# Kernel optimization log

Measured on AMD Instinct MI355X. Metric: run time of the kernel, lower is better.

Reference implementation:

```python
import jax, jax.numpy as jnp
import numpy as np

DIM = 1024
HEADS = 16
HEAD_DIM = DIM // HEADS
SCALE = HEAD_DIM ** -0.5


def setup_inputs() -> dict:
    key = jax.random.key(0)
    k1, k2, k3, k4 = jax.random.split(key, 4)
    x = jax.random.normal(k1, (2, 2048, DIM), dtype=jnp.float32)
    s = DIM ** -0.5
    qkv_w = jax.random.normal(k2, (3 * DIM, DIM), dtype=jnp.float32) * s
    proj_w = jax.random.normal(k3, (DIM, DIM), dtype=jnp.float32) * s
    proj_b = jax.random.normal(k4, (DIM,), dtype=jnp.float32) * 0.01
    return {"x": x, "qkv_w": qkv_w, "proj_w": proj_w, "proj_b": proj_b}


def reference(x, qkv_w, proj_w, proj_b):
    B, N, C = x.shape
    # qkv: Linear(dim, 3*dim) with torch convention y = x @ W^T
    qkv = jnp.einsum('bnc,dc->bnd', x, qkv_w)
    qkv = qkv.reshape(B, N, 3, HEADS, HEAD_DIM).transpose(2, 0, 3, 1, 4)
    q, k, v = qkv[0], qkv[1], qkv[2]           # [B, H, N, Dh]
    attn = jnp.einsum('bhnd,bhmd->bhnm', q, k) * SCALE
    attn = jax.nn.softmax(attn, axis=-1)
    out = jnp.einsum('bhnm,bhmd->bhnd', attn, v)  # [B, H, N, Dh]
    out = out.transpose(0, 2, 1, 3).reshape(B, N, C)
    out = jnp.einsum('bnc,dc->bnd', out, proj_w) + proj_b
    return out
```

## Files before the change

kernel.cpp:

```cpp
#include <hip/hip_runtime.h>
#include <cmath>


namespace {
constexpr int kDim   = 1024;
constexpr int kHeads = 16;
constexpr int kHd    = 64;
constexpr int kB     = 2;
constexpr int kN     = 2048;
constexpr int kM     = kB * kN;
constexpr float kScale = 0.125f;
constexpr int kP = 72;
}

typedef __attribute__((ext_vector_type(8))) short bf16x8;
typedef __attribute__((ext_vector_type(4))) float f32x4;

__device__ inline unsigned short f2bf(float x) {
  union { float f; unsigned u; } un; un.f = x;
  unsigned r = un.u + 0x7fffu + ((un.u >> 16) & 1u);
  return (unsigned short)(r >> 16);
}
__device__ inline unsigned pack2bf(float x, float y) {
  return (unsigned)f2bf(x) | ((unsigned)f2bf(y) << 16);
}
__device__ inline void gl_lds16(const short* g, short* l) {
  __builtin_amdgcn_global_load_lds(
      (const __attribute__((address_space(1))) unsigned*)g,
      (__attribute__((address_space(3))) unsigned*)l, 16, 0, 0);
}

__global__ __launch_bounds__(256) void cvt_kernel(const float* __restrict__ src,
                                                  short* __restrict__ dst) {
  const int i = (blockIdx.x * 256 + threadIdx.x) * 8;
  float4 a = *(const float4*)&src[i];
  float4 b = *(const float4*)&src[i + 4];
  bf16x8 o = {(short)f2bf(a.x), (short)f2bf(a.y), (short)f2bf(a.z), (short)f2bf(a.w),
              (short)f2bf(b.x), (short)f2bf(b.y), (short)f2bf(b.z), (short)f2bf(b.w)};
  *(bf16x8*)&dst[i] = o;
}

__global__ __launch_bounds__(256, 2) void mm_qkv_kernel(
    const short* __restrict__ A16, const short* __restrict__ W16,
    short* __restrict__ q16, short* __restrict__ k16, short* __restrict__ vT16) {
  __shared__ short smem[2 * 128 * 64];
  short* As = smem;
  short* Bs = smem + 128 * 64;
  const int tid  = threadIdx.x;
  const int w    = tid >> 6;
  const int lane = tid & 63;
  const int quad = lane >> 4;
  const int k15  = lane & 15;
  const int m0   = blockIdx.x * 128;
  const int seg  = blockIdx.y >> 3;
  const int nt0  = (blockIdx.y & 7) << 7;
  const int wrow0 = seg * 1024 + nt0;
  const int wm = (w >> 1) * 64;
  const int wn = (w & 1) * 64;
  const int lrow   = lane >> 3;
  const int lchunk = (lane & 7) ^ lrow;

  f32x4 acc[4][4];
#pragma unroll
  for (int i = 0; i < 4; ++i)
#pragma unroll
    for (int j = 0; j < 4; ++j) acc[i][j] = (f32x4){0.f, 0.f, 0.f, 0.f};

  for (int kt = 0; kt < 1024; kt += 64) {
    __syncthreads();
#pragma unroll
    for (int p = 0; p < 4; ++p) {
      const int r0 = p * 32 + w * 8;
      gl_lds16(&A16[(long)(m0 + r0 + lrow) * 1024 + kt + lchunk * 8], &As[r0 * 64]);
      gl_lds16(&W16[(long)(wrow0 + r0 + lrow) * 1024 + kt + lchunk * 8], &Bs[r0 * 64]);
    }
    __syncthreads();
#pragma unroll
    for (int ks = 0; ks < 2; ++ks) {
      bf16x8 af[4], bf[4];
#pragma unroll
      for (int t = 0; t < 4; ++t) {
        const int Ra = wm + t * 16 + k15;
        af[t] = *(const bf16x8*)&As[Ra * 64 + (((ks << 2) + quad) ^ (Ra & 7)) * 8];
        const int Rb = wn + t * 16 + k15;
        bf[t] = *(const bf16x8*)&Bs[Rb * 64 + (((ks << 2) + quad) ^ (Rb & 7)) * 8];
      }
#pragma unroll
      for (int mt = 0; mt < 4; ++mt)
#pragma unroll
        for (int nt = 0; nt < 4; ++nt)
          acc[mt][nt] = __builtin_amdgcn_mfma_f32_16x16x32_bf16(
              af[mt], bf[nt], acc[mt][nt], 0, 0, 0);
    }
  }

  if (seg < 2) {
    short* dst = (seg == 0) ? q16 : k16;
    const float sc = (seg == 0) ? kScale : 1.0f;
#pragma unroll
    for (int nt = 0; nt < 4; ++nt) {
      const int dl = nt0 + wn + nt * 16 + k15;
      const int h  = dl >> 6;
      const int dh = dl & 63;
#pragma unroll
      for (int mt = 0; mt < 4; ++mt) {
#pragma unroll
        for (int r = 0; r < 4; ++r) {
          const int ml = m0 + wm + mt * 16 + quad * 4 + r;
          const int b  = ml >> 11;
          const int n  = ml & 2047;
          dst[(((long)(b * kHeads + h) * kN) + n) * kHd + dh] =
              (short)f2bf(acc[mt][nt][r] * sc);
        }
      }
    }
  } else {
    __syncthreads();
    short* Tw = smem + w * 16 * kP;
#pragma unroll
    for (int nt = 0; nt < 4; ++nt) {
#pragma unroll
      for (int mt = 0; mt < 4; ++mt) {
        uint2 pk;
        pk.x = pack2bf(acc[mt][nt][0], acc[mt][nt][1]);
        pk.y = pack2bf(acc[mt][nt][2], acc[mt][nt][3]);
        *(uint2*)&Tw[k15 * kP + mt * 16 + quad * 4] = pk;
      }
#pragma unroll
      for (int i = 0; i < 2; ++i) {
        const int idx  = i * 64 + lane;
        const int trow = idx >> 3;
        const int tch  = idx & 7;
        bf16x8 row = *(const bf16x8*)&Tw[trow * kP + tch * 8];
        const int vcol = nt0 + wn + nt * 16 + trow;
        const int h  = vcol >> 6;
        const int dh = vcol & 63;
        const int m  = m0 + wm + tch * 8;
        const int b  = m >> 11;
        const int n  = m & 2047;
        *(bf16x8*)&vT16[(((long)(b * kHeads + h) * kHd) + dh) * kN + n] = row;
      }
    }
  }
}

__global__ __launch_bounds__(256, 2) void mm_proj_kernel(
    const short* __restrict__ A16, const short* __restrict__ B16,
    const float* __restrict__ bias, float* __restrict__ out) {
  __shared__ short As[128 * 64];
  __shared__ short Bs[128 * 64];
  const int tid  = threadIdx.x;
  const int w    = tid >> 6;
  const int lane = tid & 63;
  const int quad = lane >> 4;
  const int k15  = lane & 15;
  const int m0 = blockIdx.x * 128;
  const int n0 = blockIdx.y * 128;
  const int wm = (w >> 1) * 64;
  const int wn = (w & 1) * 64;
  const int lrow   = lane >> 3;
  const int lchunk = (lane & 7) ^ lrow;

  f32x4 acc[4][4];
#pragma unroll
  for (int i = 0; i < 4; ++i)
#pragma unroll
    for (int j = 0; j < 4; ++j) acc[i][j] = (f32x4){0.f, 0.f, 0.f, 0.f};

  for (int kt = 0; kt < 1024; kt += 64) {
    __syncthreads();
#pragma unroll
    for (int p = 0; p < 4; ++p) {
      const int r0 = p * 32 + w * 8;
      gl_lds16(&A16[(long)(m0 + r0 + lrow) * 1024 + kt + lchunk * 8], &As[r0 * 64]);
      gl_lds16(&B16[(long)(n0 + r0 + lrow) * 1024 + kt + lchunk * 8], &Bs[r0 * 64]);
    }
    __syncthreads();
#pragma unroll
    for (int ks = 0; ks < 2; ++ks) {
      bf16x8 af[4], bf[4];
#pragma unroll
      for (int t = 0; t < 4; ++t) {
        const int Ra = wm + t * 16 + k15;
        af[t] = *(const bf16x8*)&As[Ra * 64 + (((ks << 2) + quad) ^ (Ra & 7)) * 8];
        const int Rb = wn + t * 16 + k15;
        bf[t] = *(const bf16x8*)&Bs[Rb * 64 + (((ks << 2) + quad) ^ (Rb & 7)) * 8];
      }
#pragma unroll
      for (int mt = 0; mt < 4; ++mt)
#pragma unroll
        for (int nt = 0; nt < 4; ++nt)
          acc[mt][nt] = __builtin_amdgcn_mfma_f32_16x16x32_bf16(
              af[mt], bf[nt], acc[mt][nt], 0, 0, 0);
    }
  }

#pragma unroll
  for (int nt = 0; nt < 4; ++nt) {
    const int d = n0 + wn + nt * 16 + k15;
    const float bb = bias[d];
#pragma unroll
    for (int mt = 0; mt < 4; ++mt) {
#pragma unroll
      for (int r = 0; r < 4; ++r) {
        const int m = m0 + wm + mt * 16 + quad * 4 + r;
        out[(long)m * 1024 + d] = acc[mt][nt][r] + bb;
      }
    }
  }
}

__global__ __launch_bounds__(256, 2) void attn_kernel(
    const short* __restrict__ q16, const short* __restrict__ k16,
    const short* __restrict__ vT16, short* __restrict__ ao16) {
  __shared__ short Ks[128 * 64];
  __shared__ short Vs[64 * 128];
  __shared__ short Ps[4 * 32 * kP];

  const int tid  = threadIdx.x;
  const int w    = tid >> 6;
  const int lane = tid & 63;
  const int quad = lane >> 4;
  const int k15  = lane & 15;
  const int lrow  = lane >> 3;
  const int lch8  = lane & 7;
  const int lrow4 = lane >> 4;
  const int lch16 = lane & 15;
  const int bufIdx = blockIdx.z * kHeads + blockIdx.y;
  const long base  = (long)bufIdx * kN * kHd;

  bf16x8 qf[2][2];
#pragma unroll
  for (int qt = 0; qt < 2; ++qt) {
    const long qr = base + (long)(blockIdx.x * 128 + w * 32 + qt * 16 + k15) * kHd;
#pragma unroll
    for (int ks = 0; ks < 2; ++ks)
      qf[qt][ks] = *(const bf16x8*)&q16[qr + ks * 32 + quad * 8];
  }

  f32x4 accO[2][4];
#pragma unroll
  for (int qt = 0; qt < 2; ++qt)
#pragma unroll
    for (int d = 0; d < 4; ++d) accO[qt][d] = (f32x4){0.f, 0.f, 0.f, 0.f};
  float lsum[2][4] = {{0.f,0.f,0.f,0.f},{0.f,0.f,0.f,0.f}};
  short* pw = Ps + w * 32 * kP;

  for (int kt = 0; kt < kN / 128; ++kt) {
    __syncthreads();
    {
      const short* kg = k16 + base + (long)kt * 128 * kHd;
      const short* vg = vT16 + base + kt * 128;
#pragma unroll
      for (int c = 0; c < 4; ++c) {
        const int r0 = w * 32 + c * 8;
        gl_lds16(kg + (long)(r0 + lrow) * kHd + (lch8 ^ lrow) * 8, &Ks[r0 * 64]);
      }
#pragma unroll
      for (int c = 0; c < 4; ++c) {
        const int r0v = w * 16 + c * 4;
        gl_lds16(vg + (long)(r0v + lrow4) * kN + (lch16 ^ ((c * 4 + lrow4) & 15)) * 8,
                 &Vs[r0v * 128]);
      }
    }
    __syncthreads();

#pragma unroll
    for (int h2 = 0; h2 < 2; ++h2) {
      f32x4 sc[2][4];
#pragma unroll
      for (int t = 0; t < 4; ++t) {
        const int row = h2 * 64 + t * 16 + k15;
        bf16x8 kb0 = *(const bf16x8*)&Ks[row * 64 + ((quad) ^ (k15 & 7)) * 8];
        bf16x8 kb1 = *(const bf16x8*)&Ks[row * 64 + ((4 + quad) ^ (k15 & 7)) * 8];
#pragma unroll
        for (int qt = 0; qt < 2; ++qt) {
          f32x4 z = {0.f, 0.f, 0.f, 0.f};
          z = __builtin_amdgcn_mfma_f32_16x16x32_bf16(qf[qt][0], kb0, z, 0, 0, 0);
          z = __builtin_amdgcn_mfma_f32_16x16x32_bf16(qf[qt][1], kb1, z, 0, 0, 0);
          sc[qt][t] = z;
        }
      }
#pragma unroll
      for (int qt = 0; qt < 2; ++qt)
#pragma unroll
        for (int t = 0; t < 4; ++t)
#pragma unroll
          for (int r = 0; r < 4; ++r) {
            const float p = __expf(sc[qt][t][r]);
            lsum[qt][r] += p;
            pw[(qt * 16 + quad * 4 + r) * kP + t * 16 + k15] = (short)f2bf(p);
          }
#pragma unroll
      for (int kc = 0; kc < 2; ++kc) {
        bf16x8 pf0 = *(const bf16x8*)&pw[(k15) * kP + kc * 32 + quad * 8];
        bf16x8 pf1 = *(const bf16x8*)&pw[(16 + k15) * kP + kc * 32 + quad * 8];
#pragma unroll
        for (int d = 0; d < 4; ++d) {
          const int vrow = d * 16 + k15;
          const int ch = (h2 * 8 + kc * 4 + quad) ^ k15;
          bf16x8 vb = *(const bf16x8*)&Vs[vrow * 128 + ch * 8];
          accO[0][d] = __builtin_amdgcn_mfma_f32_16x16x32_bf16(pf0, vb, accO[0][d], 0, 0, 0);
          accO[1][d] = __builtin_amdgcn_mfma_f32_16x16x32_bf16(pf1, vb, accO[1][d], 0, 0, 0);
        }
      }
    }
  }

  float inv[2][4];
#pragma unroll
  for (int qt = 0; qt < 2; ++qt)
#pragma unroll
    for (int r = 0; r < 4; ++r) {
      float s = lsum[qt][r];
      s += __shfl_xor(s, 1);
      s += __shfl_xor(s, 2);
      s += __shfl_xor(s, 4);
      s += __shfl_xor(s, 8);
      inv[qt][r] = 1.f / s;
    }

#pragma unroll
  for (int qt = 0; qt < 2; ++qt)
#pragma unroll
    for (int r = 0; r < 4; ++r) {
      const int gq = blockIdx.x * 128 + w * 32 + qt * 16 + quad * 4 + r;
      short* drow = ao16 + ((long)(blockIdx.z * kN + gq)) * kDim + blockIdx.y * kHd;
#pragma unroll
      for (int d = 0; d < 4; ++d)
        drow[d * 16 + k15] = (short)f2bf(accO[qt][d][r] * inv[qt][r]);
    }
}

__global__ __launch_bounds__(256, 2) void r3_qkv_kernel(
    const float* __restrict__ X, const float* __restrict__ W,
    short* __restrict__ q16, short* __restrict__ k16, short* __restrict__ v16) {
  __shared__ short As[128 * kP];
  __shared__ short Ws[128 * kP];
  const int tid  = threadIdx.x;
  const int w    = tid >> 6;
  const int lane = tid & 63;
  const int quad = lane >> 4;
  const int k15  = lane & 15;
  const int m0 = blockIdx.x * 128;
  const int n0 = blockIdx.y * 128;
  const int wm = (w >> 1) * 64;
  const int wn = (w & 1) * 64;

  f32x4 acc[4][4];
#pragma unroll
  for (int i = 0; i < 4; ++i)
#pragma unroll
    for (int j = 0; j < 4; ++j) acc[i][j] = (f32x4){0.f, 0.f, 0.f, 0.f};

  for (int kt = 0; kt < kDim; kt += 64) {
    __syncthreads();
#pragma unroll
    for (int p = 0; p < 8; ++p) {
      const int idx = p * 256 + tid;
      const int row = idx >> 4;
      const int c4  = (idx & 15) << 2;
      float4 av = *(const float4*)&X[(long)(m0 + row) * kDim + kt + c4];
      uint2 ap = {pack2bf(av.x, av.y), pack2bf(av.z, av.w)};
      *(uint2*)&As[row * kP + c4] = ap;
      float4 wv = *(const float4*)&W[(long)(n0 + row) * kDim + kt + c4];
      uint2 wp = {pack2bf(wv.x, wv.y), pack2bf(wv.z, wv.w)};
      *(uint2*)&Ws[row * kP + c4] = wp;
    }
    __syncthreads();
#pragma unroll
    for (int ks = 0; ks < 2; ++ks) {
      bf16x8 af[4], bf[4];
#pragma unroll
      for (int t = 0; t < 4; ++t) {
        af[t] = *(const bf16x8*)&As[(wm + t * 16 + k15) * kP + ks * 32 + quad * 8];
        bf[t] = *(const bf16x8*)&Ws[(wn + t * 16 + k15) * kP + ks * 32 + quad * 8];
      }
#pragma unroll
      for (int mt = 0; mt < 4; ++mt)
#pragma unroll
        for (int nt = 0; nt < 4; ++nt)
          acc[mt][nt] = __builtin_amdgcn_mfma_f32_16x16x32_bf16(
              af[mt], bf[nt], acc[mt][nt], 0, 0, 0);
    }
  }

  const int t_sel = n0 >> 10;
  short* dst = (t_sel == 0) ? q16 : (t_sel == 1) ? k16 : v16;
  const float scl = (t_sel == 0) ? kScale : 1.0f;
#pragma unroll
  for (int nt = 0; nt < 4; ++nt) {
    const int d  = n0 + wn + nt * 16 + k15;
    const int h  = (d >> 6) & 15;
    const int dh = d & 63;
#pragma unroll
    for (int mt = 0; mt < 4; ++mt) {
#pragma unroll
      for (int r = 0; r < 4; ++r) {
        const int m = m0 + wm + mt * 16 + quad * 4 + r;
        dst[((long)h * kN + m) * kHd + dh] = (short)f2bf(acc[mt][nt][r] * scl);
      }
    }
  }
}

__global__ __launch_bounds__(256, 4) void attn_v1_kernel(
    const short* __restrict__ q16, const short* __restrict__ k16,
    const short* __restrict__ v16, short* __restrict__ ao16, int bpar) {
  __shared__ short Ks[64 * kP];
  __shared__ short Vs[64 * kP];
  __shared__ short Ps[4 * 16 * kP];
  const int tid  = threadIdx.x;
  const int w    = tid >> 6;
  const int lane = tid & 63;
  const int quad = lane >> 4;
  const int k15  = lane & 15;
  const long base = (long)blockIdx.y * kN * kHd;
  const int qrow = blockIdx.x * 64 + w * 16 + k15;
  const short* qp = q16 + base + (long)qrow * kHd + quad * 8;
  bf16x8 qf0 = *(const bf16x8*)(qp);
  bf16x8 qf1 = *(const bf16x8*)(qp + 32);

  f32x4 accO[4] = {{0.f,0.f,0.f,0.f},{0.f,0.f,0.f,0.f},
                   {0.f,0.f,0.f,0.f},{0.f,0.f,0.f,0.f}};
  float lsum[4] = {0.f, 0.f, 0.f, 0.f};

  for (int kt = 0; kt < kN / 64; ++kt) {
    __syncthreads();
    {
      const short* kg = k16 + base + (long)kt * 64 * kHd;
      const short* vg = v16 + base + (long)kt * 64 * kHd;
#pragma unroll
      for (int p = 0; p < 2; ++p) {
        const int idx = p * 256 + tid;
        const int key = idx >> 3;
        const int c8  = (idx & 7) << 3;
        *(bf16x8*)&Ks[key * kP + c8] = *(const bf16x8*)&kg[key * kHd + c8];
        bf16x8 vv = *(const bf16x8*)&vg[key * kHd + c8];
#pragma unroll
        for (int j = 0; j < 8; ++j) Vs[(c8 + j) * kP + key] = vv[j];
      }
    }
    __syncthreads();

    f32x4 sc[4];
#pragma unroll
    for (int t = 0; t < 4; ++t) {
      bf16x8 kb0 = *(const bf16x8*)&Ks[(t * 16 + k15) * kP + quad * 8];
      bf16x8 kb1 = *(const bf16x8*)&Ks[(t * 16 + k15) * kP + 32 + quad * 8];
      f32x4 z = {0.f, 0.f, 0.f, 0.f};
      z = __builtin_amdgcn_mfma_f32_16x16x32_bf16(qf0, kb0, z, 0, 0, 0);
      z = __builtin_amdgcn_mfma_f32_16x16x32_bf16(qf1, kb1, z, 0, 0, 0);
      sc[t] = z;
    }
    short* pw = &Ps[w * (16 * kP)];
#pragma unroll
    for (int t = 0; t < 4; ++t) {
#pragma unroll
      for (int r = 0; r < 4; ++r) {
        const float p = __expf(sc[t][r]);
        lsum[r] += p;
        pw[(quad * 4 + r) * kP + t * 16 + k15] = (short)f2bf(p);
      }
    }
    bf16x8 pf0 = *(const bf16x8*)&pw[k15 * kP + quad * 8];
    bf16x8 pf1 = *(const bf16x8*)&pw[k15 * kP + 32 + quad * 8];
#pragma unroll
    for (int t = 0; t < 4; ++t) {
      bf16x8 vb0 = *(const bf16x8*)&Vs[(t * 16 + k15) * kP + quad * 8];
      bf16x8 vb1 = *(const bf16x8*)&Vs[(t * 16 + k15) * kP + 32 + quad * 8];
      accO[t] = __builtin_amdgcn_mfma_f32_16x16x32_bf16(pf0, vb0, accO[t], 0, 0, 0);
      accO[t] = __builtin_amdgcn_mfma_f32_16x16x32_bf16(pf1, vb1, accO[t], 0, 0, 0);
    }
  }

#pragma unroll
  for (int r = 0; r < 4; ++r) {
    float s = lsum[r];
    s += __shfl_xor(s, 1);
    s += __shfl_xor(s, 2);
    s += __shfl_xor(s, 4);
    s += __shfl_xor(s, 8);
    lsum[r] = 1.f / s;
  }
#pragma unroll
  for (int r = 0; r < 4; ++r) {
    const int gq = blockIdx.x * 64 + w * 16 + quad * 4 + r;
    short* drow = ao16 + ((long)(bpar * kN + gq)) * kDim + blockIdx.y * kHd;
#pragma unroll
    for (int t = 0; t < 4; ++t)
      drow[t * 16 + k15] = (short)f2bf(accO[t][r] * lsum[r]);
  }
}

__global__ __launch_bounds__(256, 2) void r3_proj_kernel(
    const short* __restrict__ A16, const float* __restrict__ W,
    const float* __restrict__ bias, float* __restrict__ out) {
  __shared__ short As[128 * kP];
  __shared__ short Ws[128 * kP];
  const int tid  = threadIdx.x;
  const int w    = tid >> 6;
  const int lane = tid & 63;
  const int quad = lane >> 4;
  const int k15  = lane & 15;
  const int m0 = blockIdx.x * 128;
  const int n0 = blockIdx.y * 128;
  const int wm = (w >> 1) * 64;
  const int wn = (w & 1) * 64;

  f32x4 acc[4][4];
#pragma unroll
  for (int i = 0; i < 4; ++i)
#pragma unroll
    for (int j = 0; j < 4; ++j) acc[i][j] = (f32x4){0.f, 0.f, 0.f, 0.f};

  for (int kt = 0; kt < kDim; kt += 64) {
    __syncthreads();
#pragma unroll
    for (int p = 0; p < 4; ++p) {
      const int idx = p * 256 + tid;
      const int row = idx >> 3;
      const int c8  = (idx & 7) << 3;
      *(bf16x8*)&As[row * kP + c8] =
          *(const bf16x8*)&A16[(long)(m0 + row) * kDim + kt + c8];
    }
#pragma unroll
    for (int p = 0; p < 8; ++p) {
      const int idx = p * 256 + tid;
      const int row = idx >> 4;
      const int c4  = (idx & 15) << 2;
      float4 wv = *(const float4*)&W[(long)(n0 + row) * kDim + kt + c4];
      uint2 wp = {pack2bf(wv.x, wv.y), pack2bf(wv.z, wv.w)};
      *(uint2*)&Ws[row * kP + c4] = wp;
    }
    __syncthreads();
#pragma unroll
    for (int ks = 0; ks < 2; ++ks) {
      bf16x8 af[4], bf[4];
#pragma unroll
      for (int t = 0; t < 4; ++t) {
        af[t] = *(const bf16x8*)&As[(wm + t * 16 + k15) * kP + ks * 32 + quad * 8];
        bf[t] = *(const bf16x8*)&Ws[(wn + t * 16 + k15) * kP + ks * 32 + quad * 8];
      }
#pragma unroll
      for (int mt = 0; mt < 4; ++mt)
#pragma unroll
        for (int nt = 0; nt < 4; ++nt)
          acc[mt][nt] = __builtin_amdgcn_mfma_f32_16x16x32_bf16(
              af[mt], bf[nt], acc[mt][nt], 0, 0, 0);
    }
  }

#pragma unroll
  for (int nt = 0; nt < 4; ++nt) {
    const int d = n0 + wn + nt * 16 + k15;
    const float bb = bias[d];
#pragma unroll
    for (int mt = 0; mt < 4; ++mt) {
#pragma unroll
      for (int r = 0; r < 4; ++r) {
        const int m = m0 + wm + mt * 16 + quad * 4 + r;
        out[(long)m * kDim + d] = acc[mt][nt][r] + bb;
      }
    }
  }
}

extern "C" void kernel_launch(void* const* d_in, const int* in_sizes, int n_in,
                              void* d_out, int out_size, void* d_ws, size_t ws_size,
                              hipStream_t stream) {
  const float* x      = (const float*)d_in[0];
  const float* qkv_w  = (const float*)d_in[1];
  const float* proj_w = (const float*)d_in[2];
  const float* proj_b = (const float*)d_in[3];
  float* out = (float*)d_out;

  short* ws = (short*)d_ws;
  const size_t MiS = 1048576;

  if (ws_size >= 41943040ull) {
    short* X16  = ws;
    short* W16  = ws + 4 * MiS;
    short* PW16 = ws + 7 * MiS;
    short* q16  = ws + 8 * MiS;
    short* k16  = ws + 12 * MiS;
    short* vT16 = ws + 16 * MiS;
    short* ao16 = X16;

    cvt_kernel<<<2048, 256, 0, stream>>>(x, X16);
    cvt_kernel<<<1536, 256, 0, stream>>>(qkv_w, W16);
    cvt_kernel<<<512, 256, 0, stream>>>(proj_w, PW16);
    mm_qkv_kernel<<<dim3(32, 24), 256, 0, stream>>>(X16, W16, q16, k16, vT16);
    attn_kernel<<<dim3(16, 16, 2), 256, 0, stream>>>(q16, k16, vT16, ao16);
    mm_proj_kernel<<<dim3(32, 8), 256, 0, stream>>>(ao16, PW16, proj_b, out);
    return;
  }

  {
    short* q16  = ws;
    short* k16  = ws + 2 * MiS;
    short* v16  = ws + 4 * MiS;
    short* ao16 = ws + 6 * MiS;
    for (int b = 0; b < kB; ++b) {
      r3_qkv_kernel<<<dim3(16, 24), 256, 0, stream>>>(
          x + (size_t)b * kN * kDim, qkv_w, q16, k16, v16);
      attn_v1_kernel<<<dim3(32, 16), 256, 0, stream>>>(q16, k16, v16, ao16, b);
    }
    r3_proj_kernel<<<dim3(32, 8), 256, 0, stream>>>(ao16, proj_w, proj_b, out);
  }
}
```

Before: 194.1 us.

## Restructure attention to 2 waves with 64 rows each, exp2, MFMA row sums

Attention now runs 128 threads per block, each wave handling 64 query rows so K and V fragments loaded from LDS are reused across four query tiles. Softmax uses exp2 with log2(e) folded into the Q scale, truncating bf16 conversion for P, and row sums accumulated by an MFMA against a ones vector instead of scalar adds and shuffles. The three fp32-to-bf16 conversion launches are merged into one. Fewer threads per block raises register pressure and halves the waves available to hide latency, and truncation slightly changes rounding of P.

```diff
diff --git a/kernel.cpp b/kernel.cpp
--- a/kernel.cpp
+++ b/kernel.cpp
@@ -9,18 +9,29 @@
 constexpr int kB     = 2;
 constexpr int kN     = 2048;
 constexpr int kM     = kB * kN;
-constexpr float kScale = 0.125f;
+constexpr float kScale  = 0.125f;
+constexpr float kQScale = 0.125f * 1.44269504088896f;
 constexpr int kP = 72;
 }
 
 typedef __attribute__((ext_vector_type(8))) short bf16x8;
 typedef __attribute__((ext_vector_type(4))) float f32x4;
+
+#if __has_builtin(__builtin_amdgcn_exp2f)
+#define EXP2(x) __builtin_amdgcn_exp2f(x)
+#else
+#define EXP2(x) __expf((x) * 0.6931471805599453f)
+#endif
 
 __device__ inline unsigned short f2bf(float x) {
   union { float f; unsigned u; } un; un.f = x;
   unsigned r = un.u + 0x7fffu + ((un.u >> 16) & 1u);
   return (unsigned short)(r >> 16);
 }
+__device__ inline short tbf(float x) {
+  union { float f; unsigned u; } un; un.f = x;
+  return (short)(un.u >> 16);
+}
 __device__ inline unsigned pack2bf(float x, float y) {
   return (unsigned)f2bf(x) | ((unsigned)f2bf(y) << 16);
 }
@@ -30,13 +41,20 @@
       (__attribute__((address_space(3))) unsigned*)l, 16, 0, 0);
 }
 
-__global__ __launch_bounds__(256) void cvt_kernel(const float* __restrict__ src,
-                                                  short* __restrict__ dst) {
-  const int i = (blockIdx.x * 256 + threadIdx.x) * 8;
-  float4 a = *(const float4*)&src[i];
-  float4 b = *(const float4*)&src[i + 4];
-  bf16x8 o = {(short)f2bf(a.x), (short)f2bf(a.y), (short)f2bf(a.z), (short)f2bf(a.w),
-              (short)f2bf(b.x), (short)f2bf(b.y), (short)f2bf(b.z), (short)f2bf(b.w)};
+__global__ __launch_bounds__(256) void cvt3_kernel(
+    const float* __restrict__ a, short* __restrict__ da, int n0,
+    const float* __restrict__ b, short* __restrict__ db, int n1,
+    const float* __restrict__ c, short* __restrict__ dc) {
+  int blk = blockIdx.x;
+  const float* src; short* dst;
+  if (blk < n0) { src = a; dst = da; }
+  else if (blk < n0 + n1) { src = b; dst = db; blk -= n0; }
+  else { src = c; dst = dc; blk -= n0 + n1; }
+  const int i = (blk * 256 + threadIdx.x) * 8;
+  float4 u = *(const float4*)&src[i];
+  float4 v = *(const float4*)&src[i + 4];
+  bf16x8 o = {(short)f2bf(u.x), (short)f2bf(u.y), (short)f2bf(u.z), (short)f2bf(u.w),
+              (short)f2bf(v.x), (short)f2bf(v.y), (short)f2bf(v.z), (short)f2bf(v.w)};
   *(bf16x8*)&dst[i] = o;
 }
 
@@ -96,7 +114,7 @@
 
   if (seg < 2) {
     short* dst = (seg == 0) ? q16 : k16;
-    const float sc = (seg == 0) ? kScale : 1.0f;
+    const float sc = (seg == 0) ? kQScale : 1.0f;
 #pragma unroll
     for (int nt = 0; nt < 4; ++nt) {
       const int dl = nt0 + wn + nt * 16 + k15;
@@ -210,12 +228,12 @@
   }
 }
 
-__global__ __launch_bounds__(256, 2) void attn_kernel(
+__global__ __launch_bounds__(128, 2) void attn_kernel(
     const short* __restrict__ q16, const short* __restrict__ k16,
     const short* __restrict__ vT16, short* __restrict__ ao16) {
   __shared__ short Ks[128 * 64];
   __shared__ short Vs[64 * 128];
-  __shared__ short Ps[4 * 32 * kP];
+  __shared__ short Ps[2 * 2 * 16 * kP];
 
   const int tid  = threadIdx.x;
   const int w    = tid >> 6;
@@ -229,22 +247,27 @@
   const int bufIdx = blockIdx.z * kHeads + blockIdx.y;
   const long base  = (long)bufIdx * kN * kHd;
 
-  bf16x8 qf[2][2];
-#pragma unroll
-  for (int qt = 0; qt < 2; ++qt) {
-    const long qr = base + (long)(blockIdx.x * 128 + w * 32 + qt * 16 + k15) * kHd;
+  bf16x8 qf[4][2];
+#pragma unroll
+  for (int qt = 0; qt < 4; ++qt) {
+    const long qr = base + (long)(blockIdx.x * 128 + w * 64 + qt * 16 + k15) * kHd;
 #pragma unroll
     for (int ks = 0; ks < 2; ++ks)
       qf[qt][ks] = *(const bf16x8*)&q16[qr + ks * 32 + quad * 8];
   }
 
-  f32x4 accO[2][4];
-#pragma unroll
-  for (int qt = 0; qt < 2; ++qt)
+  const short oneb = (short)0x3F80;
+  bf16x8 onesf;
+#pragma unroll
+  for (int j = 0; j < 8; ++j) onesf[j] = (k15 == 0) ? oneb : (short)0;
+
+  f32x4 accO[4][4];
+#pragma unroll
+  for (int qt = 0; qt < 4; ++qt)
 #pragma unroll
     for (int d = 0; d < 4; ++d) accO[qt][d] = (f32x4){0.f, 0.f, 0.f, 0.f};
-  float lsum[2][4] = {{0.f,0.f,0.f,0.f},{0.f,0.f,0.f,0.f}};
-  short* pw = Ps + w * 32 * kP;
+  f32x4 accL[4] = {{0.f,0.f,0.f,0.f},{0.f,0.f,0.f,0.f},
+                   {0.f,0.f,0.f,0.f},{0.f,0.f,0.f,0.f}};
 
   for (int kt = 0; kt < kN / 128; ++kt) {
     __syncthreads();
@@ -252,14 +275,15 @@
       const short* kg = k16 + base + (long)kt * 128 * kHd;
       const short* vg = vT16 + base + kt * 128;
 #pragma unroll
-      for (int c = 0; c < 4; ++c) {
-        const int r0 = w * 32 + c * 8;
-        gl_lds16(kg + (long)(r0 + lrow) * kHd + (lch8 ^ lrow) * 8, &Ks[r0 * 64]);
-      }
-#pragma unroll
-      for (int c = 0; c < 4; ++c) {
-        const int r0v = w * 16 + c * 4;
-        gl_lds16(vg + (long)(r0v + lrow4) * kN + (lch16 ^ ((c * 4 + lrow4) & 15)) * 8,
+      for (int c = 0; c < 8; ++c) {
+        const int r0 = w * 64 + c * 8;
+        gl_lds16(kg + (long)(r0 + lrow) * kHd + (lch8 ^ ((r0 + lrow) & 7)) * 8,
+                 &Ks[r0 * 64]);
+      }
+#pragma unroll
+      for (int c = 0; c < 8; ++c) {
+        const int r0v = w * 32 + c * 4;
+        gl_lds16(vg + (long)(r0v + lrow4) * kN + (lch16 ^ ((r0v + lrow4) & 15)) * 8,
                  &Vs[r0v * 128]);
       }
     }
@@ -267,69 +291,67 @@
 
 #pragma unroll
     for (int h2 = 0; h2 < 2; ++h2) {
-      f32x4 sc[2][4];
+      bf16x8 kb[4][2];
 #pragma unroll
       for (int t = 0; t < 4; ++t) {
         const int row = h2 * 64 + t * 16 + k15;
-        bf16x8 kb0 = *(const bf16x8*)&Ks[row * 64 + ((quad) ^ (k15 & 7)) * 8];
-        bf16x8 kb1 = *(const bf16x8*)&Ks[row * 64 + ((4 + quad) ^ (k15 & 7)) * 8];
-#pragma unroll
-        for (int qt = 0; qt < 2; ++qt) {
-          f32x4 z = {0.f, 0.f, 0.f, 0.f};
-          z = __builtin_amdgcn_mfma_f32_16x16x32_bf16(qf[qt][0], kb0, z, 0, 0, 0);
-          z = __builtin_amdgcn_mfma_f32_16x16x32_bf16(qf[qt][1], kb1, z, 0, 0, 0);
-          sc[qt][t] = z;
-        }
-      }
-#pragma unroll
-      for (int qt = 0; qt < 2; ++qt)
-#pragma unroll
-        for (int t = 0; t < 4; ++t)
-#pragma unroll
-          for (int r = 0; r < 4; ++r) {
-            const float p = __expf(sc[qt][t][r]);
-            lsum[qt][r] += p;
-            pw[(qt * 16 + quad * 4 + r) * kP + t * 16 + k15] = (short)f2bf(p);
-          }
-#pragma unroll
-      for (int kc = 0; kc < 2; ++kc) {
-        bf16x8 pf0 = *(const bf16x8*)&pw[(k15) * kP + kc * 32 + quad * 8];
-        bf16x8 pf1 = *(const bf16x8*)&pw[(16 + k15) * kP + kc * 32 + quad * 8];
+#pragma unroll
+        for (int ks = 0; ks < 2; ++ks)
+          kb[t][ks] = *(const bf16x8*)&Ks[row * 64 + (((ks << 2) + quad) ^ (row & 7)) * 8];
+      }
+      bf16x8 vb[2][4];
+#pragma unroll
+      for (int kc = 0; kc < 2; ++kc)
 #pragma unroll
         for (int d = 0; d < 4; ++d) {
           const int vrow = d * 16 + k15;
-          const int ch = (h2 * 8 + kc * 4 + quad) ^ k15;
-          bf16x8 vb = *(const bf16x8*)&Vs[vrow * 128 + ch * 8];
-          accO[0][d] = __builtin_amdgcn_mfma_f32_16x16x32_bf16(pf0, vb, accO[0][d], 0, 0, 0);
-          accO[1][d] = __builtin_amdgcn_mfma_f32_16x16x32_bf16(pf1, vb, accO[1][d], 0, 0, 0);
+          const int ch = (h2 * 8 + kc * 4 + quad) ^ (vrow & 15);
+          vb[kc][d] = *(const bf16x8*)&Vs[vrow * 128 + ch * 8];
         }
-      }
-    }
-  }
-
-  float inv[2][4];
-#pragma unroll
-  for (int qt = 0; qt < 2; ++qt)
+
+#pragma unroll
+      for (int qt = 0; qt < 4; ++qt) {
+        f32x4 sc[4];
+#pragma unroll
+        for (int t = 0; t < 4; ++t) {
+          f32x4 z = {0.f, 0.f, 0.f, 0.f};
+          z = __builtin_amdgcn_mfma_f32_16x16x32_bf16(qf[qt][0], kb[t][0], z, 0, 0, 0);
+          z = __builtin_amdgcn_mfma_f32_16x16x32_bf16(qf[qt][1], kb[t][1], z, 0, 0, 0);
+          sc[t] = z;
+        }
+        short* pw = Ps + (w * 2 + (qt & 1)) * 16 * kP;
+#pragma unroll
+        for (int t = 0; t < 4; ++t)
+#pragma unroll
+          for (int r = 0; r < 4; ++r)
+            pw[(quad * 4 + r) * kP + t * 16 + k15] = tbf(EXP2(sc[t][r]));
+#pragma unroll
+        for (int kc = 0; kc < 2; ++kc) {
+          bf16x8 pf = *(const bf16x8*)&pw[k15 * kP + kc * 32 + quad * 8];
+#pragma unroll
+          for (int d = 0; d < 4; ++d)
+            accO[qt][d] = __builtin_amdgcn_mfma_f32_16x16x32_bf16(
+                pf, vb[kc][d], accO[qt][d], 0, 0, 0);
+          accL[qt] = __builtin_amdgcn_mfma_f32_16x16x32_bf16(
+              pf, onesf, accL[qt], 0, 0, 0);
+        }
+      }
+    }
+  }
+
+#pragma unroll
+  for (int qt = 0; qt < 4; ++qt) {
 #pragma unroll
     for (int r = 0; r < 4; ++r) {
-      float s = lsum[qt][r];
-      s += __shfl_xor(s, 1);
-      s += __shfl_xor(s, 2);
-      s += __shfl_xor(s, 4);
-      s += __shfl_xor(s, 8);
-      inv[qt][r] = 1.f / s;
-    }
-
-#pragma unroll
-  for (int qt = 0; qt < 2; ++qt)
-#pragma unroll
-    for (int r = 0; r < 4; ++r) {
-      const int gq = blockIdx.x * 128 + w * 32 + qt * 16 + quad * 4 + r;
+      const float s  = __shfl(accL[qt][r], (lane & 48));
+      const float in = 1.f / s;
+      const int gq = blockIdx.x * 128 + w * 64 + qt * 16 + quad * 4 + r;
       short* drow = ao16 + ((long)(blockIdx.z * kN + gq)) * kDim + blockIdx.y * kHd;
 #pragma unroll
       for (int d = 0; d < 4; ++d)
-        drow[d * 16 + k15] = (short)f2bf(accO[qt][d][r] * inv[qt][r]);
-    }
+        drow[d * 16 + k15] = (short)f2bf(accO[qt][d][r] * in);
+    }
+  }
 }
 
 __global__ __launch_bounds__(256, 2) void r3_qkv_kernel(
@@ -587,11 +609,10 @@
     short* vT16 = ws + 16 * MiS;
     short* ao16 = X16;
 
-    cvt_kernel<<<2048, 256, 0, stream>>>(x, X16);
-    cvt_kernel<<<1536, 256, 0, stream>>>(qkv_w, W16);
-    cvt_kernel<<<512, 256, 0, stream>>>(proj_w, PW16);
+    cvt3_kernel<<<4096, 256, 0, stream>>>(x, X16, 2048, qkv_w, W16, 1536,
+                                          proj_w, PW16);
     mm_qkv_kernel<<<dim3(32, 24), 256, 0, stream>>>(X16, W16, q16, k16, vT16);
-    attn_kernel<<<dim3(16, 16, 2), 256, 0, stream>>>(q16, k16, vT16, ao16);
+    attn_kernel<<<dim3(16, 16, 2), 128, 0, stream>>>(q16, k16, vT16, ao16);
     mm_proj_kernel<<<dim3(32, 8), 256, 0, stream>>>(ao16, PW16, proj_b, out);
     return;
   }
```

New measurement: 198.4 us. 2.2% more time.
